# Performance work log

Measured on AMD Instinct MI355X. Metric: run time of the kernel, lower is better.

## Reference

```python
import jax, jax.numpy as jnp
import numpy as np

D_MODEL = 512
NH_ATTN = 8
D_STATE = 64
HEADDIM = 128
D_INNER = 2 * D_MODEL          # 1024
NHEADS = D_INNER // HEADDIM    # 8
CONV_K = 4
CONV_DIM = D_INNER + 2 * D_STATE            # 1152
D_IN_PROJ = 2 * D_INNER + 2 * D_STATE + NHEADS  # 2184
B, S, M = 2, 2048, 1024
EPS = 1e-5


def setup_inputs() -> dict:
    key = jax.random.key(0)
    ks = jax.random.split(key, 10)
    s = 0.02
    return {
        'x': jax.random.normal(ks[0], (B, S, D_MODEL), dtype=jnp.float32),
        'memory': jax.random.normal(ks[1], (B, M, D_MODEL), dtype=jnp.float32),
        'pad_mask': jnp.ones((B, S, 1), dtype=jnp.float32),
        'ln1_g': jnp.ones((D_MODEL,)), 'ln1_b': jnp.zeros((D_MODEL,)),
        'ln2_g': jnp.ones((D_MODEL,)), 'ln2_b': jnp.zeros((D_MODEL,)),
        'W_in': jax.random.normal(ks[2], (D_IN_PROJ, D_MODEL)) * s,
        'conv_w': jax.random.normal(ks[3], (CONV_DIM, 1, CONV_K)) * s,
        'conv_b': jnp.zeros((CONV_DIM,)),
        'dt_bias': jnp.log(jnp.expm1(jax.random.uniform(ks[4], (NHEADS,), minval=0.001, maxval=0.1))),
        'A_log': jnp.log(jnp.arange(1, NHEADS + 1, dtype=jnp.float32)),
        'D_skip': jnp.ones((NHEADS,)),
        'rms_w': jnp.ones((D_INNER,)),
        'W_out': jax.random.normal(ks[5], (D_MODEL, D_INNER)) * s,
        'Wqkv': jax.random.normal(ks[6], (3 * D_MODEL, D_MODEL)) * s,
        'bqkv': jnp.zeros((3 * D_MODEL,)),
        'Wo': jax.random.normal(ks[7], (D_MODEL, D_MODEL)) * s,
        'bo': jnp.zeros((D_MODEL,)),
    }


def _layernorm(x, g, b):
    m = jnp.mean(x, axis=-1, keepdims=True)
    v = jnp.mean((x - m) ** 2, axis=-1, keepdims=True)
    return (x - m) * jax.lax.rsqrt(v + EPS) * g + b


def _mamba(x, W_in, conv_w, conv_b, dt_bias, A_log, D_skip, rms_w, W_out):
    b, s, _ = x.shape
    zxbcdt = x @ W_in.T                                     # [b,s,2184]
    z, xBC, dt = jnp.split(zxbcdt, [D_INNER, D_INNER + CONV_DIM], axis=-1)
    # causal depthwise conv over time on (x, B, C)
    xt = jnp.transpose(xBC, (0, 2, 1))                      # [b,C,s]
    xt = jax.lax.conv_general_dilated(
        xt, conv_w, (1,), [(CONV_K - 1, 0)],
        feature_group_count=CONV_DIM,
        dimension_numbers=('NCH', 'OIH', 'NCH'))
    xBC = jax.nn.silu(jnp.transpose(xt, (0, 2, 1)) + conv_b)
    xs, Bm, Cm = jnp.split(xBC, [D_INNER, D_INNER + D_STATE], axis=-1)
    dt = jax.nn.softplus(dt + dt_bias)                      # [b,s,H]
    A = -jnp.exp(A_log)                                     # [H]
    xh = xs.reshape(b, s, NHEADS, HEADDIM)                  # [b,s,H,P]

    def step(h, inps):
        dt_t, B_t, C_t, x_t = inps                          # [b,H],[b,N],[b,N],[b,H,P]
        decay = jnp.exp(dt_t * A)                           # [b,H]
        h = h * decay[..., None, None] + (dt_t[..., None, None] * x_t[..., None]) * B_t[:, None, None, :]
        y = jnp.einsum('bhpn,bn->bhp', h, C_t)
        return h, y

    h0 = jnp.zeros((b, NHEADS, HEADDIM, D_STATE), dtype=x.dtype)
    _, ys = jax.lax.scan(step, h0, (dt.transpose(1, 0, 2), Bm.transpose(1, 0, 2),
                                    Cm.transpose(1, 0, 2), xh.transpose(1, 0, 2, 3)))
    y = ys.transpose(1, 0, 2, 3) + D_skip[None, None, :, None] * xh
    y = y.reshape(b, s, D_INNER) * jax.nn.silu(z)           # gated
    y = y * jax.lax.rsqrt(jnp.mean(y * y, axis=-1, keepdims=True) + EPS) * rms_w
    return y @ W_out.T


def _cross_attn(q_in, memory, Wqkv, bqkv, Wo, bo):
    b, s, _ = q_in.shape
    m = memory.shape[1]
    dh = D_MODEL // NH_ATTN
    q = (q_in @ Wqkv[:D_MODEL].T + bqkv[:D_MODEL]).reshape(b, s, NH_ATTN, dh)
    k = (memory @ Wqkv[D_MODEL:2 * D_MODEL].T + bqkv[D_MODEL:2 * D_MODEL]).reshape(b, m, NH_ATTN, dh)
    v = (memory @ Wqkv[2 * D_MODEL:].T + bqkv[2 * D_MODEL:]).reshape(b, m, NH_ATTN, dh)
    scores = jnp.einsum('bqhd,bkhd->bhqk', q, k) / jnp.sqrt(jnp.asarray(dh, q.dtype))
    p = jax.nn.softmax(scores, axis=-1)
    out = jnp.einsum('bhqk,bkhd->bqhd', p, v).reshape(b, s, D_MODEL)
    return out @ Wo.T + bo


def reference(x, memory, pad_mask, ln1_g, ln1_b, ln2_g, ln2_b, W_in, conv_w, conv_b,
              dt_bias, A_log, D_skip, rms_w, W_out, Wqkv, bqkv, Wo, bo):
    residual = x
    xn = _layernorm(x, ln1_g, ln1_b) * pad_mask
    x = residual + _mamba(xn, W_in, conv_w, conv_b, dt_bias, A_log, D_skip, rms_w, W_out)
    h = _layernorm(x, ln2_g, ln2_b)
    x = x + _cross_attn(h, memory, Wqkv, bqkv, Wo, bo)
    return x
```

## Files before the change

kernel.cpp:

```cpp
#include <hip/hip_runtime.h>
#include <hip/hip_bf16.h>

typedef __hip_bfloat16 bf16;
typedef short v8s __attribute__((ext_vector_type(8)));
typedef short v4s __attribute__((ext_vector_type(4)));
typedef float v4f __attribute__((ext_vector_type(4)));

__device__ __forceinline__ void gll16(const bf16* g, bf16* l) {
    __builtin_amdgcn_global_load_lds(
        (const __attribute__((address_space(1))) unsigned int*)g,
        (__attribute__((address_space(3))) unsigned int*)l, 16, 0, 0);
}
__device__ __forceinline__ float bf2f(short s) {
    return __uint_as_float(((unsigned int)(unsigned short)s) << 16);
}
__device__ __forceinline__ short f2bfs(float f) {
    return (short)__bfloat16_as_ushort(__float2bfloat16(f));
}

__global__ __launch_bounds__(256) void pre_kernel(
    const float* __restrict__ x, const float* __restrict__ g,
    const float* __restrict__ bt, const float* __restrict__ mask,
    bf16* __restrict__ xn,
    const float* __restrict__ W_in, const float* __restrict__ W_out,
    const float* __restrict__ Wqkv, const float* __restrict__ Wo,
    const float* __restrict__ mem,
    bf16* __restrict__ Winb, bf16* __restrict__ Woutb, bf16* __restrict__ Wqkvb,
    bf16* __restrict__ Wob, bf16* __restrict__ memb)
{
    int tid = threadIdx.x;
    if (blockIdx.x < 4096) {
        int row = blockIdx.x;
        const float* xr = x + (size_t)row * 512;
        float v0 = xr[tid], v1 = xr[tid + 256];
        float s = v0 + v1, ss = v0 * v0 + v1 * v1;
        #pragma unroll
        for (int o = 32; o; o >>= 1) { s += __shfl_xor(s, o); ss += __shfl_xor(ss, o); }
        __shared__ float l1[4], l2[4];
        if ((tid & 63) == 0) { l1[tid >> 6] = s; l2[tid >> 6] = ss; }
        __syncthreads();
        s = l1[0] + l1[1] + l1[2] + l1[3];
        ss = l2[0] + l2[1] + l2[2] + l2[3];
        float mean = s * (1.f / 512.f);
        float var = ss * (1.f / 512.f) - mean * mean;
        float rs = rsqrtf(var + 1e-5f);
        float mk = mask[row];
        xn[(size_t)row * 512 + tid] =
            __float2bfloat16(((v0 - mean) * rs * g[tid] + bt[tid]) * mk);
        xn[(size_t)row * 512 + tid + 256] =
            __float2bfloat16(((v1 - mean) * rs * g[tid + 256] + bt[tid + 256]) * mk);
        return;
    }
    int i = (blockIdx.x - 4096) * 256 + tid;
    const int E0 = 2184 * 512;
    const int E1 = E0 + 524288;
    const int E2 = E1 + 786432;
    const int E3 = E2 + 262144;
    const int E4 = E3 + 1048576;
    if (i < E0) {
        Winb[i] = __float2bfloat16(W_in[i]);
    } else if (i < E1) {
        int j = i - E0; Woutb[j] = __float2bfloat16(W_out[j]);
    } else if (i < E2) {
        int j = i - E1; Wqkvb[j] = __float2bfloat16(Wqkv[j]);
    } else if (i < E3) {
        int j = i - E2; Wob[j] = __float2bfloat16(Wo[j]);
    } else if (i < E4) {
        int j = i - E3; memb[j] = __float2bfloat16(mem[j]);
    }
}

__global__ __launch_bounds__(256) void ln_kernel(
    const bf16* __restrict__ x, const float* __restrict__ g,
    const float* __restrict__ bt, bf16* __restrict__ out)
{
    int row = blockIdx.x, tid = threadIdx.x;
    const bf16* xr = x + (size_t)row * 512;
    unsigned int pk = *(const unsigned int*)(xr + tid * 2);
    float v0 = bf2f((short)(pk & 0xffff));
    float v1 = bf2f((short)(pk >> 16));
    float s = v0 + v1, ss = v0 * v0 + v1 * v1;
    #pragma unroll
    for (int o = 32; o; o >>= 1) { s += __shfl_xor(s, o); ss += __shfl_xor(ss, o); }
    __shared__ float l1[4], l2[4];
    if ((tid & 63) == 0) { l1[tid >> 6] = s; l2[tid >> 6] = ss; }
    __syncthreads();
    s = l1[0] + l1[1] + l1[2] + l1[3];
    ss = l2[0] + l2[1] + l2[2] + l2[3];
    float mean = s * (1.f / 512.f);
    float var = ss * (1.f / 512.f) - mean * mean;
    float rs = rsqrtf(var + 1e-5f);
    int i0 = tid * 2;
    unsigned int po =
        (unsigned int)(unsigned short)f2bfs((v0 - mean) * rs * g[i0] + bt[i0]) |
        ((unsigned int)(unsigned short)f2bfs((v1 - mean) * rs * g[i0 + 1] + bt[i0 + 1]) << 16);
    *(unsigned int*)(out + (size_t)row * 512 + i0) = po;
}

__global__ __launch_bounds__(256) void gemm_in(
    const bf16* __restrict__ A, const bf16* __restrict__ W, bf16* __restrict__ C)
{
    __shared__ bf16 lA[2][64 * 32];
    __shared__ bf16 lB[2][128 * 32];
    int bm = blockIdx.x * 64, bn = blockIdx.y * 128;
    int tid = threadIdx.x, lane = tid & 63, wv = tid >> 6;
    int wc = wv * 32;
    int lr15 = lane & 15, l4 = lane >> 4, lk8 = (lane >> 4) * 8;

    v4f acc[4][2] = {};
    int sr = tid >> 2, sc = (tid & 3) * 8;
    const bf16* Abase = A + (size_t)(bm + sr) * 512 + sc;
    const bf16* Wbase = W + (size_t)(bn + sr) * 512 + sc;

    int cur = 0;
    gll16(Abase, &lA[0][tid * 8]);
    gll16(Wbase, &lB[0][tid * 8]);
    gll16(Wbase + (size_t)64 * 512, &lB[0][tid * 8 + 2048]);
    __syncthreads();
    for (int t = 0; t < 16; ++t) {
        if (t + 1 < 16) {
            int k0 = (t + 1) * 32;
            gll16(Abase + k0, &lA[cur ^ 1][tid * 8]);
            gll16(Wbase + k0, &lB[cur ^ 1][tid * 8]);
            gll16(Wbase + (size_t)64 * 512 + k0, &lB[cur ^ 1][tid * 8 + 2048]);
        }
        v8s af[4], bfr[2];
        #pragma unroll
        for (int mi = 0; mi < 4; ++mi)
            af[mi] = *(const v8s*)&lA[cur][(mi * 16 + lr15) * 32 + lk8];
        #pragma unroll
        for (int ni = 0; ni < 2; ++ni)
            bfr[ni] = *(const v8s*)&lB[cur][(wc + ni * 16 + lr15) * 32 + lk8];
        #pragma unroll
        for (int mi = 0; mi < 4; ++mi)
            #pragma unroll
            for (int ni = 0; ni < 2; ++ni)
                acc[mi][ni] = __builtin_amdgcn_mfma_f32_16x16x32_bf16(
                    af[mi], bfr[ni], acc[mi][ni], 0, 0, 0);
        __syncthreads();
        cur ^= 1;
    }
    #pragma unroll
    for (int mi = 0; mi < 4; ++mi) {
        #pragma unroll
        for (int ni = 0; ni < 2; ++ni) {
            int col = bn + wc + ni * 16 + lr15;
            if (col < 2184) {
                #pragma unroll
                for (int r = 0; r < 4; ++r) {
                    int row = bm + mi * 16 + l4 * 4 + r;
                    C[(size_t)row * 2184 + col] = __float2bfloat16(acc[mi][ni][r]);
                }
            }
        }
    }
}

__global__ __launch_bounds__(256) void gemm64(
    const bf16* __restrict__ Aall, const bf16* __restrict__ Wall,
    const float* __restrict__ bias, const void* __restrict__ resid,
    void* __restrict__ Cout,
    int M, int N, int K, int ldA, int ldW, int ldC,
    long sA1, long sA2, long sW1, long sW2, long sC1, long sC2,
    int zdiv, int outbf16, int residbf16, bf16* __restrict__ vTout)
{
    __shared__ bf16 lA[2][64 * 32];
    __shared__ bf16 lB[2][64 * 32];
    int z = blockIdx.z;
    int zb = z / zdiv, zh = z - zb * zdiv;
    const bf16* A = Aall + zb * sA1 + zh * sA2;
    const bf16* W = Wall + zb * sW1 + zh * sW2;
    long coff = zb * sC1 + zh * sC2;

    int bm = blockIdx.x * 64, bn = blockIdx.y * 64;
    int tid = threadIdx.x, lane = tid & 63, wv = tid >> 6;
    int wr = (wv >> 1) * 32, wc = (wv & 1) * 32;
    int lr15 = lane & 15, lk8 = (lane >> 4) * 8;

    v4f acc[2][2] = {};
    int sr = tid >> 2, sc = (tid & 3) * 8;
    const bf16* Abase = A + (size_t)(bm + sr) * ldA + sc;
    const bf16* Wbase = W + (size_t)(bn + sr) * ldW + sc;

    int nt = K >> 5, cur = 0;
    gll16(Abase, &lA[0][tid * 8]);
    gll16(Wbase, &lB[0][tid * 8]);
    __syncthreads();
    for (int t = 0; t < nt; ++t) {
        if (t + 1 < nt) {
            int k0 = (t + 1) * 32;
            gll16(Abase + k0, &lA[cur ^ 1][tid * 8]);
            gll16(Wbase + k0, &lB[cur ^ 1][tid * 8]);
        }
        v8s a0 = *(const v8s*)&lA[cur][(wr + lr15) * 32 + lk8];
        v8s a1 = *(const v8s*)&lA[cur][(wr + 16 + lr15) * 32 + lk8];
        v8s b0 = *(const v8s*)&lB[cur][(wc + lr15) * 32 + lk8];
        v8s b1 = *(const v8s*)&lB[cur][(wc + 16 + lr15) * 32 + lk8];
        acc[0][0] = __builtin_amdgcn_mfma_f32_16x16x32_bf16(a0, b0, acc[0][0], 0, 0, 0);
        acc[0][1] = __builtin_amdgcn_mfma_f32_16x16x32_bf16(a0, b1, acc[0][1], 0, 0, 0);
        acc[1][0] = __builtin_amdgcn_mfma_f32_16x16x32_bf16(a1, b0, acc[1][0], 0, 0, 0);
        acc[1][1] = __builtin_amdgcn_mfma_f32_16x16x32_bf16(a1, b1, acc[1][1], 0, 0, 0);
        __syncthreads();
        cur ^= 1;
    }
    int r0 = bm + wr + (lane >> 4) * 4;
    int c0 = bn + wc + lr15;
    #pragma unroll
    for (int mi = 0; mi < 2; ++mi) {
        #pragma unroll
        for (int ni = 0; ni < 2; ++ni) {
            int col = c0 + ni * 16;
            if (col < N) {
                float bv = bias ? bias[col] : 0.f;
                float vals[4];
                #pragma unroll
                for (int r = 0; r < 4; ++r) {
                    int row = r0 + mi * 16 + r;
                    long idx = coff + (long)row * ldC + col;
                    float v = acc[mi][ni][r] + bv;
                    if (resid)
                        v += residbf16 ? bf2f(((const short*)resid)[idx])
                                       : ((const float*)resid)[idx];
                    vals[r] = v;
                    if (outbf16) ((bf16*)Cout)[idx] = __float2bfloat16(v);
                    else ((float*)Cout)[idx] = v;
                }
                if (vTout && col >= 512) {
                    int d = col - 512;
                    int row0 = r0 + mi * 16;
                    int bb = row0 >> 10, m0 = row0 & 1023;
                    v4s pk;
                    #pragma unroll
                    for (int r = 0; r < 4; ++r) pk[r] = f2bfs(vals[r]);
                    *(v4s*)(vTout + (((size_t)(bb * 8 + (d >> 6)) * 64 + (d & 63))
                                     * 1024 + m0)) = pk;
                }
            }
        }
    }
}

__global__ __launch_bounds__(256) void qkv_proj(
    const bf16* __restrict__ hb, const bf16* __restrict__ memb,
    const bf16* __restrict__ Wqkvb, const float* __restrict__ bqkv,
    bf16* __restrict__ qb, bf16* __restrict__ kvb, bf16* __restrict__ vTout)
{
    __shared__ bf16 lA[2][64 * 32];
    __shared__ bf16 lB[2][64 * 32];
    const bf16* A; const bf16* W; const float* bias; bf16* C;
    int bm, bn, ldA, ldC;
    bf16* vT = nullptr;
    if (blockIdx.z == 0) {
        A = hb; W = Wqkvb; bias = bqkv; C = qb;
        bm = blockIdx.x * 64; bn = blockIdx.y * 64;
        ldA = 512; ldC = 512;
    } else {
        int id = blockIdx.y * 64 + blockIdx.x;
        A = memb; W = Wqkvb + 512 * 512; bias = bqkv + 512; C = kvb;
        bm = (id & 31) * 64; bn = (id >> 5) * 64;
        ldA = 512; ldC = 1024;
        vT = vTout;
    }
    int tid = threadIdx.x, lane = tid & 63, wv = tid >> 6;
    int wr = (wv >> 1) * 32, wc = (wv & 1) * 32;
    int lr15 = lane & 15, lk8 = (lane >> 4) * 8;

    v4f acc[2][2] = {};
    int sr = tid >> 2, sc = (tid & 3) * 8;
    const bf16* Abase = A + (size_t)(bm + sr) * ldA + sc;
    const bf16* Wbase = W + (size_t)(bn + sr) * 512 + sc;

    int cur = 0;
    gll16(Abase, &lA[0][tid * 8]);
    gll16(Wbase, &lB[0][tid * 8]);
    __syncthreads();
    for (int t = 0; t < 16; ++t) {
        if (t + 1 < 16) {
            int k0 = (t + 1) * 32;
            gll16(Abase + k0, &lA[cur ^ 1][tid * 8]);
            gll16(Wbase + k0, &lB[cur ^ 1][tid * 8]);
        }
        v8s a0 = *(const v8s*)&lA[cur][(wr + lr15) * 32 + lk8];
        v8s a1 = *(const v8s*)&lA[cur][(wr + 16 + lr15) * 32 + lk8];
        v8s b0 = *(const v8s*)&lB[cur][(wc + lr15) * 32 + lk8];
        v8s b1 = *(const v8s*)&lB[cur][(wc + 16 + lr15) * 32 + lk8];
        acc[0][0] = __builtin_amdgcn_mfma_f32_16x16x32_bf16(a0, b0, acc[0][0], 0, 0, 0);
        acc[0][1] = __builtin_amdgcn_mfma_f32_16x16x32_bf16(a0, b1, acc[0][1], 0, 0, 0);
        acc[1][0] = __builtin_amdgcn_mfma_f32_16x16x32_bf16(a1, b0, acc[1][0], 0, 0, 0);
        acc[1][1] = __builtin_amdgcn_mfma_f32_16x16x32_bf16(a1, b1, acc[1][1], 0, 0, 0);
        __syncthreads();
        cur ^= 1;
    }
    int r0 = bm + wr + (lane >> 4) * 4;
    int c0 = bn + wc + lr15;
    #pragma unroll
    for (int mi = 0; mi < 2; ++mi) {
        #pragma unroll
        for (int ni = 0; ni < 2; ++ni) {
            int col = c0 + ni * 16;
            float bv = bias[col];
            float vals[4];
            #pragma unroll
            for (int r = 0; r < 4; ++r) {
                int row = r0 + mi * 16 + r;
                float v = acc[mi][ni][r] + bv;
                vals[r] = v;
                C[(size_t)row * ldC + col] = __float2bfloat16(v);
            }
            if (vT && col >= 512) {
                int d = col - 512;
                int row0 = r0 + mi * 16;
                int bb = row0 >> 10, m0 = row0 & 1023;
                v4s pk;
                #pragma unroll
                for (int r = 0; r < 4; ++r) pk[r] = f2bfs(vals[r]);
                *(v4s*)(vT + (((size_t)(bb * 8 + (d >> 6)) * 64 + (d & 63))
                              * 1024 + m0)) = pk;
            }
        }
    }
}

__global__ __launch_bounds__(256) void flash_attn(
    const bf16* __restrict__ qb, const bf16* __restrict__ kvb,
    const bf16* __restrict__ vT, bf16* __restrict__ attn)
{
    __shared__ bf16 lK[2][128 * 64];
    __shared__ bf16 lV[2][64 * 128];
    __shared__ bf16 lP[4][16 * 128];
    int z = blockIdx.z;
    int b = z >> 3, h = z & 7;
    int q0 = blockIdx.x * 64;
    int tid = threadIdx.x, lane = tid & 63, wv = tid >> 6;
    int l15 = lane & 15, l4 = lane >> 4, l7 = lane & 7;

    const bf16* Qg = qb + (size_t)(b * 2048 + q0) * 512 + h * 64;
    const bf16* Kg = kvb + (size_t)b * 1024 * 1024 + h * 64;
    const bf16* Vg = vT + (size_t)z * 64 * 1024;

    v8s af[2];
    #pragma unroll
    for (int ks = 0; ks < 2; ++ks)
        af[ks] = *(const v8s*)(Qg + (size_t)(wv * 16 + l15) * 512 + (ks * 4 + l4) * 8);

    #pragma unroll
    for (int pass = 0; pass < 4; ++pass) {
        int s = pass * 256 + tid;
        int kr = s >> 3, kc = s & 7;
        gll16(Kg + (size_t)kr * 1024 + ((kc ^ (kr & 7)) << 3), &lK[0][s * 8]);
        int vr = s >> 4, vc = s & 15;
        int vsw = (vc & 8) | ((vc & 7) ^ (vr & 7));
        gll16(Vg + (size_t)vr * 1024 + (vsw << 3), &lV[0][s * 8]);
    }
    __syncthreads();

    v4f o[4] = {};
    v4f l_run = (v4f){0.f, 0.f, 0.f, 0.f};
    bf16* lPw = &lP[wv][0];

    int cur = 0;
    #pragma unroll 1
    for (int t = 0; t < 8; ++t) {
        if (t + 1 < 8) {
            int k0n = (t + 1) * 128;
            #pragma unroll
            for (int pass = 0; pass < 4; ++pass) {
                int s = pass * 256 + tid;
                int kr = s >> 3, kc = s & 7;
                gll16(Kg + (size_t)(k0n + kr) * 1024 + ((kc ^ (kr & 7)) << 3),
                      &lK[cur ^ 1][s * 8]);
                int vr = s >> 4, vc = s & 15;
                int vsw = (vc & 8) | ((vc & 7) ^ (vr & 7));
                gll16(Vg + (size_t)vr * 1024 + k0n + (vsw << 3), &lV[cur ^ 1][s * 8]);
            }
        }
        v4f s_acc[8];
        #pragma unroll
        for (int kn = 0; kn < 8; ++kn) {
            s_acc[kn] = (v4f){0.f, 0.f, 0.f, 0.f};
            #pragma unroll
            for (int ks = 0; ks < 2; ++ks) {
                v8s kv = *(const v8s*)&lK[cur][(kn * 16 + l15) * 64 +
                                               (((ks * 4 + l4) ^ l7) << 3)];
                s_acc[kn] = __builtin_amdgcn_mfma_f32_16x16x32_bf16(
                    af[ks], kv, s_acc[kn], 0, 0, 0);
            }
        }
        v4f rs = {0.f, 0.f, 0.f, 0.f};
        #pragma unroll
        for (int kn = 0; kn < 8; ++kn)
            #pragma unroll
            for (int r = 0; r < 4; ++r) {
                float pv = __expf(0.125f * s_acc[kn][r]);
                s_acc[kn][r] = pv;
                rs[r] += pv;
            }
        #pragma unroll
        for (int off = 8; off >= 1; off >>= 1)
            #pragma unroll
            for (int r = 0; r < 4; ++r)
                rs[r] += __shfl_xor(rs[r], off);
        #pragma unroll
        for (int r = 0; r < 4; ++r)
            l_run[r] += rs[r];
        #pragma unroll
        for (int kn = 0; kn < 8; ++kn)
            #pragma unroll
            for (int r = 0; r < 4; ++r) {
                int row = l4 * 4 + r;
                int col = kn * 16 + l15;
                int c = col >> 3;
                int csw = (c & 8) | ((c & 7) ^ (row & 7));
                lPw[row * 128 + (csw << 3) + (col & 7)] =
                    __float2bfloat16(s_acc[kn][r]);
            }
        #pragma unroll
        for (int ni = 0; ni < 4; ++ni)
            #pragma unroll
            for (int ks = 0; ks < 4; ++ks) {
                int ck = ks * 4 + l4;
                int psw = (ck & 8) | ((ck & 7) ^ l7);
                v8s pv = *(const v8s*)&lPw[l15 * 128 + (psw << 3)];
                v8s vv = *(const v8s*)&lV[cur][(ni * 16 + l15) * 128 + (psw << 3)];
                o[ni] = __builtin_amdgcn_mfma_f32_16x16x32_bf16(
                    pv, vv, o[ni], 0, 0, 0);
            }
        __syncthreads();
        cur ^= 1;
    }
    v4f inv;
    #pragma unroll
    for (int r = 0; r < 4; ++r) inv[r] = 1.f / l_run[r];
    #pragma unroll
    for (int ni = 0; ni < 4; ++ni)
        #pragma unroll
        for (int r = 0; r < 4; ++r) {
            int row = q0 + wv * 16 + l4 * 4 + r;
            int col = h * 64 + ni * 16 + l15;
            attn[(size_t)(b * 2048 + row) * 512 + col] =
                __float2bfloat16(o[ni][r] * inv[r]);
        }
}

__global__ __launch_bounds__(256) void conv_dt(
    const bf16* __restrict__ zx, const float* __restrict__ cw,
    const float* __restrict__ cb, bf16* __restrict__ out,
    const float* __restrict__ dt_bias, const float* __restrict__ A_log,
    float* __restrict__ dtb, float* __restrict__ decb)
{
    int tid = threadIdx.x;
    if (blockIdx.x >= 576) {
        int i = (blockIdx.x - 576) * 256 + tid;
        if (i >= 32768) return;
        int h = i & 7, row = i >> 3;
        float d = bf2f(((const short*)zx)[(size_t)row * 2184 + 2176 + h]) + dt_bias[h];
        float sp = d > 20.f ? d : log1pf(expf(d));
        dtb[i] = sp;
        decb[i] = expf(-expf(A_log[h]) * sp);
        return;
    }
    int idx = blockIdx.x * 256 + tid;
    int c4 = (idx % 288) * 4;
    int tb = (idx / 288) % 256;
    int b  = idx / (288 * 256);
    int t0 = tb * 8;
    const bf16* base = zx + (size_t)b * 2048 * 2184 + 1024 + c4;
    bf16* ob = out + ((size_t)(b * 2048 + t0)) * 1152 + c4;

    float wt[4][4];
    #pragma unroll
    for (int k = 0; k < 4; ++k)
        #pragma unroll
        for (int j = 0; j < 4; ++j) wt[j][k] = cw[(c4 + k) * 4 + j];
    v4f bias = *(const v4f*)(cb + c4);

    v4f r[11];
    #pragma unroll
    for (int j = 0; j < 11; ++j) {
        int ts = t0 - 3 + j;
        if (ts >= 0) {
            v4s raw = *(const v4s*)(base + (size_t)ts * 2184);
            #pragma unroll
            for (int k = 0; k < 4; ++k) r[j][k] = bf2f(raw[k]);
        } else r[j] = (v4f){0.f, 0.f, 0.f, 0.f};
    }
    #pragma unroll
    for (int t = 0; t < 8; ++t) {
        v4f acc = bias;
        #pragma unroll
        for (int k = 0; k < 4; ++k)
            acc[k] += wt[0][k] * r[t][k] + wt[1][k] * r[t + 1][k]
                    + wt[2][k] * r[t + 2][k] + wt[3][k] * r[t + 3][k];
        v4s res;
        #pragma unroll
        for (int k = 0; k < 4; ++k) {
            float v = acc[k] / (1.f + expf(-acc[k]));
            res[k] = f2bfs(v);
        }
        *(v4s*)(ob + (size_t)t * 1152) = res;
    }
}

__global__ __launch_bounds__(256) void scan_p1(
    const bf16* __restrict__ conv, const float* __restrict__ dtb,
    const float* __restrict__ decb, const float* __restrict__ A_log,
    bf16* __restrict__ slocal, float* __restrict__ cdec)
{
    int chunk = blockIdx.x, bh = blockIdx.y;
    int b = bh >> 3, h = bh & 7;
    int tid = threadIdx.x;
    int wv = tid >> 6, lane = tid & 63;
    int nh = lane >> 5, psub = lane & 31;
    int p = wv * 32 + psub;
    __shared__ bf16 lxb[64][128];
    __shared__ float lB[64][64];
    __shared__ float ldt[64], ldec[64];
    const bf16* cb_ = conv + (size_t)b * 2048 * 1152;
    int t0 = chunk * 64;
    #pragma unroll
    for (int pass = 0; pass < 4; ++pass) {
        int s = pass * 256 + tid;
        int row = s >> 4, c8 = (s & 15) * 8;
        *(v8s*)&lxb[row][c8] =
            *(const v8s*)(cb_ + (size_t)(t0 + row) * 1152 + h * 128 + c8);
    }
    #pragma unroll
    for (int pass = 0; pass < 2; ++pass) {
        int s = pass * 256 + tid;
        int row = s >> 3, c8 = (s & 7) * 8;
        v8s raw = *(const v8s*)(cb_ + (size_t)(t0 + row) * 1152 + 1024 + c8);
        v4f lo, hi;
        #pragma unroll
        for (int j = 0; j < 4; ++j) { lo[j] = bf2f(raw[j]); hi[j] = bf2f(raw[j + 4]); }
        *(v4f*)&lB[row][c8] = lo;
        *(v4f*)&lB[row][c8 + 4] = hi;
    }
    if (tid < 64) {
        int ri = (b * 2048 + t0 + tid) * 8 + h;
        ldt[tid] = dtb[ri]; ldec[tid] = decb[ri];
    }
    __syncthreads();
    v4f hs[8] = {};
    float sdt = 0.f;
    #pragma unroll 2
    for (int t = 0; t < 64; ++t) {
        float dtv = ldt[t], dec = ldec[t];
        float c1 = dtv * bf2f(*(const short*)&lxb[t][p]);
        const v4f* Bp = (const v4f*)&lB[t][nh * 32];
        #pragma unroll
        for (int i = 0; i < 8; ++i) hs[i] = hs[i] * dec + Bp[i] * c1;
        sdt += dtv;
    }
    if (tid == 0) cdec[bh * 32 + chunk] = expf(-expf(A_log[h]) * sdt);
    bf16* S = slocal + ((size_t)bh * 32 + chunk) * 8192;
    #pragma unroll
    for (int i = 0; i < 8; ++i)
        #pragma unroll
        for (int j = 0; j < 4; ++j)
            S[(nh * 32 + i * 4 + j) * 128 + p] = __float2bfloat16(hs[i][j]);
}

__global__ __launch_bounds__(256) void scan_comb(
    const bf16* __restrict__ slocal, const float* __restrict__ cdec,
    bf16* __restrict__ hinit)
{
    int e = blockIdx.x * 256 + threadIdx.x;
    int bh = e >> 12, np2 = e & 4095;
    size_t base = (size_t)bh * 262144 + (size_t)np2 * 2;
    const float* cd = cdec + bh * 32;
    float h0 = 0.f, h1 = 0.f;
    for (int c = 0; c < 32; ++c) {
        size_t idx = base + (size_t)c * 8192;
        unsigned int raw = *(const unsigned int*)(slocal + idx);
        unsigned int pk = (unsigned int)(unsigned short)f2bfs(h0) |
                          ((unsigned int)(unsigned short)f2bfs(h1) << 16);
        *(unsigned int*)(hinit + idx) = pk;
        float cdv = cd[c];
        h0 = h0 * cdv + bf2f((short)(raw & 0xffff));
        h1 = h1 * cdv + bf2f((short)(raw >> 16));
    }
}

__global__ __launch_bounds__(256) void scan_p3(
    const bf16* __restrict__ conv, const float* __restrict__ dtb,
    const float* __restrict__ decb, const bf16* __restrict__ hinit,
    const float* __restrict__ Dskip, bf16* __restrict__ ybuf)
{
    int chunk = blockIdx.x, bh = blockIdx.y;
    int b = bh >> 3, h = bh & 7;
    int tid = threadIdx.x;
    int wv = tid >> 6, lane = tid & 63;
    int nh = lane >> 5, psub = lane & 31;
    int p = wv * 32 + psub;
    __shared__ bf16 lxb[64][128];
    __shared__ float lB[64][64];
    __shared__ float lC[64][64];
    __shared__ float ldt[64], ldec[64];
    const bf16* cb_ = conv + (size_t)b * 2048 * 1152;
    int t0 = chunk * 64;
    #pragma unroll
    for (int pass = 0; pass < 4; ++pass) {
        int s = pass * 256 + tid;
        int row = s >> 4, c8 = (s & 15) * 8;
        *(v8s*)&lxb[row][c8] =
            *(const v8s*)(cb_ + (size_t)(t0 + row) * 1152 + h * 128 + c8);
    }
    #pragma unroll
    for (int pass = 0; pass < 2; ++pass) {
        int s = pass * 256 + tid;
        int row = s >> 3, c8 = (s & 7) * 8;
        v8s rawB = *(const v8s*)(cb_ + (size_t)(t0 + row) * 1152 + 1024 + c8);
        v8s rawC = *(const v8s*)(cb_ + (size_t)(t0 + row) * 1152 + 1088 + c8);
        v4f lo, hi;
        #pragma unroll
        for (int j = 0; j < 4; ++j) { lo[j] = bf2f(rawB[j]); hi[j] = bf2f(rawB[j + 4]); }
        *(v4f*)&lB[row][c8] = lo;
        *(v4f*)&lB[row][c8 + 4] = hi;
        #pragma unroll
        for (int j = 0; j < 4; ++j) { lo[j] = bf2f(rawC[j]); hi[j] = bf2f(rawC[j + 4]); }
        *(v4f*)&lC[row][c8] = lo;
        *(v4f*)&lC[row][c8 + 4] = hi;
    }
    if (tid < 64) {
        int ri = (b * 2048 + t0 + tid) * 8 + h;
        ldt[tid] = dtb[ri]; ldec[tid] = decb[ri];
    }
    __syncthreads();
    v4f hs[8];
    const bf16* H = hinit + ((size_t)bh * 32 + chunk) * 8192;
    #pragma unroll
    for (int i = 0; i < 8; ++i)
        #pragma unroll
        for (int j = 0; j < 4; ++j)
            hs[i][j] = __bfloat162float(H[(nh * 32 + i * 4 + j) * 128 + p]);
    float Dk = Dskip[h];
    #pragma unroll 2
    for (int t = 0; t < 64; ++t) {
        float dtv = ldt[t], dec = ldec[t];
        float xv = bf2f(*(const short*)&lxb[t][p]);
        float c1 = dtv * xv;
        const v4f* Bp = (const v4f*)&lB[t][nh * 32];
        const v4f* Cp = (const v4f*)&lC[t][nh * 32];
        v4f ya = {0.f, 0.f, 0.f, 0.f};
        #pragma unroll
        for (int i = 0; i < 8; ++i) {
            hs[i] = hs[i] * dec + Bp[i] * c1;
            ya += hs[i] * Cp[i];
        }
        float part = ya[0] + ya[1] + ya[2] + ya[3];
        part += __shfl_xor(part, 32);
        if (nh == 0)
            ybuf[((size_t)(b * 2048 + t0 + t)) * 1024 + h * 128 + p] =
                __float2bfloat16(part + Dk * xv);
    }
}

__global__ __launch_bounds__(256) void gate_rms(
    const bf16* __restrict__ ybuf, const bf16* __restrict__ zx,
    const float* __restrict__ rms_w, bf16* __restrict__ out)
{
    int row = blockIdx.x, tid = threadIdx.x;
    int i0 = tid * 4;
    v4s yv = *(const v4s*)(ybuf + (size_t)row * 1024 + i0);
    v4s zv = *(const v4s*)(zx + (size_t)row * 2184 + i0);
    v4f rw = *(const v4f*)(rms_w + i0);
    float vals[4];
    float ss = 0.f;
    #pragma unroll
    for (int j = 0; j < 4; ++j) {
        float y = bf2f(yv[j]);
        float z = bf2f(zv[j]);
        float g = y * (z / (1.f + expf(-z)));
        vals[j] = g;
        ss += g * g;
    }
    #pragma unroll
    for (int o = 32; o; o >>= 1) ss += __shfl_xor(ss, o);
    __shared__ float l[4];
    if ((tid & 63) == 0) l[tid >> 6] = ss;
    __syncthreads();
    ss = l[0] + l[1] + l[2] + l[3];
    float rs = rsqrtf(ss * (1.f / 1024.f) + 1e-5f);
    v4s o4;
    #pragma unroll
    for (int j = 0; j < 4; ++j)
        o4[j] = f2bfs(vals[j] * rs * rw[j]);
    *(v4s*)(out + (size_t)row * 1024 + i0) = o4;
}

extern "C" void kernel_launch(void* const* d_in, const int* in_sizes, int n_in,
                              void* d_out, int out_size, void* d_ws, size_t ws_size,
                              hipStream_t stream) {
    (void)in_sizes; (void)n_in; (void)out_size; (void)ws_size;
    const float* x       = (const float*)d_in[0];
    const float* memory  = (const float*)d_in[1];
    const float* mask    = (const float*)d_in[2];
    const float* ln1_g   = (const float*)d_in[3];
    const float* ln1_b   = (const float*)d_in[4];
    const float* ln2_g   = (const float*)d_in[5];
    const float* ln2_b   = (const float*)d_in[6];
    const float* W_in    = (const float*)d_in[7];
    const float* conv_w  = (const float*)d_in[8];
    const float* conv_b  = (const float*)d_in[9];
    const float* dt_bias = (const float*)d_in[10];
    const float* A_log   = (const float*)d_in[11];
    const float* D_skip  = (const float*)d_in[12];
    const float* rms_w   = (const float*)d_in[13];
    const float* W_out   = (const float*)d_in[14];
    const float* Wqkv    = (const float*)d_in[15];
    const float* bqkv    = (const float*)d_in[16];
    const float* Wo      = (const float*)d_in[17];
    const float* bo      = (const float*)d_in[18];
    float* out = (float*)d_out;

    char* w = (char*)d_ws;
    bf16*  xn     = (bf16*)(w + 0);
    bf16*  Winb   = (bf16*)(w + 4194304);
    bf16*  Woutb  = (bf16*)(w + 6430720);
    bf16*  Wqkvb  = (bf16*)(w + 7479296);
    bf16*  Wob    = (bf16*)(w + 9052160);
    bf16*  memb   = (bf16*)(w + 9576448);
    bf16*  zx     = (bf16*)(w + 11673600);
    bf16*  gout   = (bf16*)(w + 29564928);
    bf16*  conv   = (bf16*)(w + 47456256);
    float* dtb    = (float*)(w + 66330624);
    float* decb   = (float*)(w + 66461696);
    bf16*  ybuf   = (bf16*)(w + 66592768);
    bf16*  slocal = (bf16*)(w + 83369984);
    bf16*  hinit  = (bf16*)(w + 91758592);
    bf16*  x2b    = (bf16*)(w + 100147200);
    bf16*  hb     = (bf16*)(w + 108535808);
    bf16*  qb     = (bf16*)(w + 112730112);
    float* cdec   = (float*)(w + 116924416);
    bf16*  kvb    = (bf16*)(w + 116928512);
    bf16*  vT     = (bf16*)(w + 121122816);
    bf16*  attn   = (bf16*)(w + 123219968);

    pre_kernel<<<18704, 256, 0, stream>>>(x, ln1_g, ln1_b, mask, xn,
                                          W_in, W_out, Wqkv, Wo, memory,
                                          Winb, Woutb, Wqkvb, Wob, memb);

    gemm_in<<<dim3(64, 18), 256, 0, stream>>>(xn, Winb, zx);

    conv_dt<<<704, 256, 0, stream>>>(zx, conv_w, conv_b, conv,
                                     dt_bias, A_log, dtb, decb);

    scan_p1<<<dim3(32, 16), 256, 0, stream>>>(conv, dtb, decb, A_log, slocal, cdec);
    scan_comb<<<256, 256, 0, stream>>>(slocal, cdec, hinit);
    scan_p3<<<dim3(32, 16), 256, 0, stream>>>(conv, dtb, decb, hinit, D_skip, ybuf);

    gate_rms<<<4096, 256, 0, stream>>>(ybuf, zx, rms_w, gout);

    gemm64<<<dim3(64, 8, 1), 256, 0, stream>>>(
        gout, Woutb, nullptr, (const void*)x, (void*)x2b,
        4096, 512, 1024, 1024, 1024, 512,
        0, 0, 0, 0, 0, 0, 1, 1, 0, nullptr);

    ln_kernel<<<4096, 256, 0, stream>>>(x2b, ln2_g, ln2_b, hb);

    qkv_proj<<<dim3(64, 8, 2), 256, 0, stream>>>(hb, memb, Wqkvb, bqkv,
                                                 qb, kvb, vT);

    flash_attn<<<dim3(32, 1, 16), 256, 0, stream>>>(qb, kvb, vT, attn);

    gemm64<<<dim3(64, 8, 1), 256, 0, stream>>>(
        attn, Wob, bo, (const void*)x2b, (void*)out,
        4096, 512, 512, 512, 512, 512,
        0, 0, 0, 0, 0, 0, 1, 0, 1, nullptr);
}
```

Baseline: 175.7 us.

## Move memory K/V projection into conv_dt kernel to overlap with conv work

```diff
diff --git a/kernel.cpp b/kernel.cpp
--- a/kernel.cpp
+++ b/kernel.cpp
@@ -240,87 +240,6 @@
     }
 }
 
-__global__ __launch_bounds__(256) void qkv_proj(
-    const bf16* __restrict__ hb, const bf16* __restrict__ memb,
-    const bf16* __restrict__ Wqkvb, const float* __restrict__ bqkv,
-    bf16* __restrict__ qb, bf16* __restrict__ kvb, bf16* __restrict__ vTout)
-{
-    __shared__ bf16 lA[2][64 * 32];
-    __shared__ bf16 lB[2][64 * 32];
-    const bf16* A; const bf16* W; const float* bias; bf16* C;
-    int bm, bn, ldA, ldC;
-    bf16* vT = nullptr;
-    if (blockIdx.z == 0) {
-        A = hb; W = Wqkvb; bias = bqkv; C = qb;
-        bm = blockIdx.x * 64; bn = blockIdx.y * 64;
-        ldA = 512; ldC = 512;
-    } else {
-        int id = blockIdx.y * 64 + blockIdx.x;
-        A = memb; W = Wqkvb + 512 * 512; bias = bqkv + 512; C = kvb;
-        bm = (id & 31) * 64; bn = (id >> 5) * 64;
-        ldA = 512; ldC = 1024;
-        vT = vTout;
-    }
-    int tid = threadIdx.x, lane = tid & 63, wv = tid >> 6;
-    int wr = (wv >> 1) * 32, wc = (wv & 1) * 32;
-    int lr15 = lane & 15, lk8 = (lane >> 4) * 8;
-
-    v4f acc[2][2] = {};
-    int sr = tid >> 2, sc = (tid & 3) * 8;
-    const bf16* Abase = A + (size_t)(bm + sr) * ldA + sc;
-    const bf16* Wbase = W + (size_t)(bn + sr) * 512 + sc;
-
-    int cur = 0;
-    gll16(Abase, &lA[0][tid * 8]);
-    gll16(Wbase, &lB[0][tid * 8]);
-    __syncthreads();
-    for (int t = 0; t < 16; ++t) {
-        if (t + 1 < 16) {
-            int k0 = (t + 1) * 32;
-            gll16(Abase + k0, &lA[cur ^ 1][tid * 8]);
-            gll16(Wbase + k0, &lB[cur ^ 1][tid * 8]);
-        }
-        v8s a0 = *(const v8s*)&lA[cur][(wr + lr15) * 32 + lk8];
-        v8s a1 = *(const v8s*)&lA[cur][(wr + 16 + lr15) * 32 + lk8];
-        v8s b0 = *(const v8s*)&lB[cur][(wc + lr15) * 32 + lk8];
-        v8s b1 = *(const v8s*)&lB[cur][(wc + 16 + lr15) * 32 + lk8];
-        acc[0][0] = __builtin_amdgcn_mfma_f32_16x16x32_bf16(a0, b0, acc[0][0], 0, 0, 0);
-        acc[0][1] = __builtin_amdgcn_mfma_f32_16x16x32_bf16(a0, b1, acc[0][1], 0, 0, 0);
-        acc[1][0] = __builtin_amdgcn_mfma_f32_16x16x32_bf16(a1, b0, acc[1][0], 0, 0, 0);
-        acc[1][1] = __builtin_amdgcn_mfma_f32_16x16x32_bf16(a1, b1, acc[1][1], 0, 0, 0);
-        __syncthreads();
-        cur ^= 1;
-    }
-    int r0 = bm + wr + (lane >> 4) * 4;
-    int c0 = bn + wc + lr15;
-    #pragma unroll
-    for (int mi = 0; mi < 2; ++mi) {
-        #pragma unroll
-        for (int ni = 0; ni < 2; ++ni) {
-            int col = c0 + ni * 16;
-            float bv = bias[col];
-            float vals[4];
-            #pragma unroll
-            for (int r = 0; r < 4; ++r) {
-                int row = r0 + mi * 16 + r;
-                float v = acc[mi][ni][r] + bv;
-                vals[r] = v;
-                C[(size_t)row * ldC + col] = __float2bfloat16(v);
-            }
-            if (vT && col >= 512) {
-                int d = col - 512;
-                int row0 = r0 + mi * 16;
-                int bb = row0 >> 10, m0 = row0 & 1023;
-                v4s pk;
-                #pragma unroll
-                for (int r = 0; r < 4; ++r) pk[r] = f2bfs(vals[r]);
-                *(v4s*)(vT + (((size_t)(bb * 8 + (d >> 6)) * 64 + (d & 63))
-                              * 1024 + m0)) = pk;
-            }
-        }
-    }
-}
-
 __global__ __launch_bounds__(256) void flash_attn(
     const bf16* __restrict__ qb, const bf16* __restrict__ kvb,
     const bf16* __restrict__ vT, bf16* __restrict__ attn)
@@ -442,13 +361,84 @@
         }
 }
 
-__global__ __launch_bounds__(256) void conv_dt(
+__global__ __launch_bounds__(256) void conv_dt_kv(
     const bf16* __restrict__ zx, const float* __restrict__ cw,
     const float* __restrict__ cb, bf16* __restrict__ out,
     const float* __restrict__ dt_bias, const float* __restrict__ A_log,
-    float* __restrict__ dtb, float* __restrict__ decb)
-{
+    float* __restrict__ dtb, float* __restrict__ decb,
+    const bf16* __restrict__ memb, const bf16* __restrict__ Wqkvb,
+    const float* __restrict__ bqkv, bf16* __restrict__ kvb,
+    bf16* __restrict__ vTout)
+{
+    __shared__ bf16 lA[2][64 * 32];
+    __shared__ bf16 lB[2][64 * 32];
     int tid = threadIdx.x;
+    if (blockIdx.x >= 704) {
+        int id = blockIdx.x - 704;
+        const bf16* A = memb;
+        const bf16* W = Wqkvb + 512 * 512;
+        const float* bias = bqkv + 512;
+        int bm = (id & 31) * 64, bn = (id >> 5) * 64;
+        int lane = tid & 63, wv = tid >> 6;
+        int wr = (wv >> 1) * 32, wc = (wv & 1) * 32;
+        int lr15 = lane & 15, lk8 = (lane >> 4) * 8;
+
+        v4f acc[2][2] = {};
+        int sr = tid >> 2, sc = (tid & 3) * 8;
+        const bf16* Abase = A + (size_t)(bm + sr) * 512 + sc;
+        const bf16* Wbase = W + (size_t)(bn + sr) * 512 + sc;
+
+        int cur = 0;
+        gll16(Abase, &lA[0][tid * 8]);
+        gll16(Wbase, &lB[0][tid * 8]);
+        __syncthreads();
+        for (int t = 0; t < 16; ++t) {
+            if (t + 1 < 16) {
+                int k0 = (t + 1) * 32;
+                gll16(Abase + k0, &lA[cur ^ 1][tid * 8]);
+                gll16(Wbase + k0, &lB[cur ^ 1][tid * 8]);
+            }
+            v8s a0 = *(const v8s*)&lA[cur][(wr + lr15) * 32 + lk8];
+            v8s a1 = *(const v8s*)&lA[cur][(wr + 16 + lr15) * 32 + lk8];
+            v8s b0 = *(const v8s*)&lB[cur][(wc + lr15) * 32 + lk8];
+            v8s b1 = *(const v8s*)&lB[cur][(wc + 16 + lr15) * 32 + lk8];
+            acc[0][0] = __builtin_amdgcn_mfma_f32_16x16x32_bf16(a0, b0, acc[0][0], 0, 0, 0);
+            acc[0][1] = __builtin_amdgcn_mfma_f32_16x16x32_bf16(a0, b1, acc[0][1], 0, 0, 0);
+            acc[1][0] = __builtin_amdgcn_mfma_f32_16x16x32_bf16(a1, b0, acc[1][0], 0, 0, 0);
+            acc[1][1] = __builtin_amdgcn_mfma_f32_16x16x32_bf16(a1, b1, acc[1][1], 0, 0, 0);
+            __syncthreads();
+            cur ^= 1;
+        }
+        int r0 = bm + wr + (lane >> 4) * 4;
+        int c0 = bn + wc + lr15;
+        #pragma unroll
+        for (int mi = 0; mi < 2; ++mi) {
+            #pragma unroll
+            for (int ni = 0; ni < 2; ++ni) {
+                int col = c0 + ni * 16;
+                float bv = bias[col];
+                float vals[4];
+                #pragma unroll
+                for (int r = 0; r < 4; ++r) {
+                    int row = r0 + mi * 16 + r;
+                    float v = acc[mi][ni][r] + bv;
+                    vals[r] = v;
+                    kvb[(size_t)row * 1024 + col] = __float2bfloat16(v);
+                }
+                if (col >= 512) {
+                    int d = col - 512;
+                    int row0 = r0 + mi * 16;
+                    int bb = row0 >> 10, m0 = row0 & 1023;
+                    v4s pk;
+                    #pragma unroll
+                    for (int r = 0; r < 4; ++r) pk[r] = f2bfs(vals[r]);
+                    *(v4s*)(vTout + (((size_t)(bb * 8 + (d >> 6)) * 64 + (d & 63))
+                                     * 1024 + m0)) = pk;
+                }
+            }
+        }
+        return;
+    }
     if (blockIdx.x >= 576) {
         int i = (blockIdx.x - 576) * 256 + tid;
         if (i >= 32768) return;
@@ -742,8 +732,9 @@
 
     gemm_in<<<dim3(64, 18), 256, 0, stream>>>(xn, Winb, zx);
 
-    conv_dt<<<704, 256, 0, stream>>>(zx, conv_w, conv_b, conv,
-                                     dt_bias, A_log, dtb, decb);
+    conv_dt_kv<<<1216, 256, 0, stream>>>(zx, conv_w, conv_b, conv,
+                                         dt_bias, A_log, dtb, decb,
+                                         memb, Wqkvb, bqkv, kvb, vT);
 
     scan_p1<<<dim3(32, 16), 256, 0, stream>>>(conv, dtb, decb, A_log, slocal, cdec);
     scan_comb<<<256, 256, 0, stream>>>(slocal, cdec, hinit);
@@ -758,8 +749,10 @@
 
     ln_kernel<<<4096, 256, 0, stream>>>(x2b, ln2_g, ln2_b, hb);
 
-    qkv_proj<<<dim3(64, 8, 2), 256, 0, stream>>>(hb, memb, Wqkvb, bqkv,
-                                                 qb, kvb, vT);
+    gemm64<<<dim3(64, 8, 1), 256, 0, stream>>>(
+        hb, Wqkvb, bqkv, nullptr, (void*)qb,
+        4096, 512, 512, 512, 512, 512,
+        0, 0, 0, 0, 0, 0, 1, 1, 0, nullptr);
 
     flash_attn<<<dim3(32, 1, 16), 256, 0, stream>>>(qb, kvb, vT, attn);
 
```

Result: no change. 178.4 us (+1.6%).
